# Performance work log

Hardware: AMD Instinct MI355X
Metric: run time of the kernel (lower is better)

Reference implementation:

```python
import jax, jax.numpy as jnp
import numpy as np

N, D, H, L, E, P = 50000, 128, 128, 3, 640000, 100000


def setup_inputs() -> dict:
    key = jax.random.key(0)
    ks = jax.random.split(key, 10)
    x = jax.random.normal(ks[0], (N, D), dtype=jnp.float32)
    ei = jax.random.randint(ks[1], (2, E), 0, N, dtype=jnp.int64)
    pos = jax.random.randint(ks[2], (2, P), 0, N, dtype=jnp.int64)
    neg = jax.random.randint(ks[3], (2, P), 0, N, dtype=jnp.int64)
    # GCN weights: layer0 is [D,H], rest [H,H]; D==H so stack as [L,H,H]
    gcn_w = jax.random.normal(ks[4], (L, H, H), dtype=jnp.float32) / np.sqrt(H)
    gcn_b = jnp.zeros((L, H), dtype=jnp.float32)
    pred_w = jax.random.normal(ks[5], (H * L, 1), dtype=jnp.float32) / np.sqrt(H * L)
    pred_b = jnp.zeros((1,), dtype=jnp.float32)
    return {"x": x, "ei": ei, "pos": pos, "neg": neg,
            "gcn_w": gcn_w, "gcn_b": gcn_b, "pred_w": pred_w, "pred_b": pred_b}


def reference(x, ei, pos, neg, gcn_w, gcn_b, pred_w, pred_b):
    n = x.shape[0]
    loops = jnp.arange(n, dtype=ei.dtype)
    src = jnp.concatenate([ei[0], loops])  # self-loops (GCNConv default)
    dst = jnp.concatenate([ei[1], loops])
    deg = jax.ops.segment_sum(jnp.ones_like(dst, dtype=x.dtype), dst, num_segments=n)
    dinv = jax.lax.rsqrt(deg)  # deg >= 1 thanks to self-loops
    coef = (dinv[src] * dinv[dst])[:, None]  # [E+N, 1] symmetric norm

    embs = []
    h = x
    for i in range(gcn_w.shape[0]):
        hw = h @ gcn_w[i]                                   # [N, H]
        agg = jax.ops.segment_sum(hw[src] * coef, dst, num_segments=n)
        h = jax.nn.relu(agg + gcn_b[i])
        embs.append(h)
    z = jnp.concatenate(embs, axis=1)                        # [N, H*L]

    def logits(e):
        return (z[e[0]] * z[e[1]]) @ pred_w + pred_b         # [P, 1]

    pos_logit = logits(pos)
    neg_logit = logits(neg)
    # BCEWithLogitsLoss with targets [1...1, 0...0], mean reduction
    total = pos_logit.shape[0] + neg_logit.shape[0]
    loss = (jnp.sum(-jax.nn.log_sigmoid(pos_logit)) +
            jnp.sum(-jax.nn.log_sigmoid(-neg_logit))) / total
    return loss
```

## Files before the change

### kernel.cpp

```cpp
#include <hip/hip_runtime.h>
#include <hip/hip_bf16.h>

#define DD 128

typedef __attribute__((ext_vector_type(8))) short short8;
typedef __attribute__((ext_vector_type(4))) float f32x4;
typedef __attribute__((ext_vector_type(2))) float f32x2;

static __device__ __forceinline__ int gtid() {
    return blockIdx.x * blockDim.x + threadIdx.x;
}

static __device__ __forceinline__ ushort f2bfu(float f) {
    __hip_bfloat16 h = __float2bfloat16(f);
    return *reinterpret_cast<ushort*>(&h);
}

static __device__ __forceinline__ unsigned int fp8e(float f) {
    unsigned int s = (__float_as_uint(f) >> 31) << 7;
    float a = fabsf(f);
    if (a < 0.015625f) return s | (unsigned int)rintf(a * 512.0f);
    unsigned int u = __float_as_uint(a);
    u += 0x0007FFFFu + ((u >> 20) & 1u);
    unsigned int e8 = (u >> 23) - 120u;
    unsigned int m = (u >> 20) & 7u;
    if (e8 > 15u || (e8 == 15u && m == 7u)) return s | 0x7Eu;
    return s | (e8 << 3) | m;
}

static __device__ __forceinline__ float fp8d(unsigned int b) {
    unsigned int t = b & 0x7Fu;
    float v = (t >= 8u) ? __uint_as_float((t << 20) + 0x3C000000u)
                        : (float)t * 0.001953125f;
    return (b & 0x80u) ? -v : v;
}

static __device__ __forceinline__ unsigned int pk8x2(float a, float b) {
#if __has_builtin(__builtin_amdgcn_cvt_pk_fp8_f32)
    return (unsigned int)__builtin_amdgcn_cvt_pk_fp8_f32(a, b, 0, false);
#else
    return fp8e(a) | (fp8e(b) << 8);
#endif
}

static __device__ __forceinline__ unsigned int pk8x4(float a, float b, float c, float d) {
#if __has_builtin(__builtin_amdgcn_cvt_pk_fp8_f32)
    int v = __builtin_amdgcn_cvt_pk_fp8_f32(a, b, 0, false);
    v = __builtin_amdgcn_cvt_pk_fp8_f32(c, d, v, true);
    return (unsigned int)v;
#else
    return fp8e(a) | (fp8e(b) << 8) | (fp8e(c) << 16) | (fp8e(d) << 24);
#endif
}

template <bool HI>
static __device__ __forceinline__ f32x2 fp8pk(unsigned int u) {
#if __has_builtin(__builtin_amdgcn_cvt_pk_f32_fp8)
    return __builtin_amdgcn_cvt_pk_f32_fp8((int)u, HI);
#else
    f32x2 r;
    unsigned int base = HI ? (u >> 16) : u;
    r[0] = fp8d(base & 0xFFu);
    r[1] = fp8d((base >> 8) & 0xFFu);
    return r;
#endif
}

#if __has_builtin(__builtin_elementwise_fma)
#define PKFMA(a, b, c) __builtin_elementwise_fma(a, b, c)
#else
static __device__ __forceinline__ f32x2 PKFMA(f32x2 a, f32x2 b, f32x2 c) {
    f32x2 r;
    r[0] = fmaf(a[0], b[0], c[0]);
    r[1] = fmaf(a[1], b[1], c[1]);
    return r;
}
#endif


__global__ void count_kernel(int* __restrict__ counts, const int* __restrict__ dst, int e) {
    int i = gtid();
    if (i < e) atomicAdd(&counts[dst[i]], 1);
}

__global__ __launch_bounds__(256) void scan_blocks(const int* __restrict__ counts,
                                                   int* __restrict__ rowptr,
                                                   int* __restrict__ partial,
                                                   float* __restrict__ dinv, int n) {
    __shared__ int s[256];
    int i = blockIdx.x * 256 + threadIdx.x;
    int v = (i < n) ? counts[i] : 0;
    if (i < n) dinv[i] = rsqrtf(1.0f + (float)v);
    s[threadIdx.x] = v;
    __syncthreads();
    for (int off = 1; off < 256; off <<= 1) {
        int t = (threadIdx.x >= off) ? s[threadIdx.x - off] : 0;
        __syncthreads();
        s[threadIdx.x] += t;
        __syncthreads();
    }
    if (i < n) rowptr[i] = s[threadIdx.x] - v;
    if (threadIdx.x == 255) partial[blockIdx.x] = s[255];
}

__global__ __launch_bounds__(256) void scan_partials(int* __restrict__ partial,
                                                     int* __restrict__ partial2, int nb) {
    __shared__ int s[256];
    int v = (threadIdx.x < nb) ? partial[threadIdx.x] : 0;
    s[threadIdx.x] = v;
    __syncthreads();
    for (int off = 1; off < 256; off <<= 1) {
        int t = (threadIdx.x >= off) ? s[threadIdx.x - off] : 0;
        __syncthreads();
        s[threadIdx.x] += t;
        __syncthreads();
    }
    partial2[threadIdx.x] = s[threadIdx.x] - v;
}

__global__ __launch_bounds__(256) void add_offsets(int* __restrict__ rowptr,
                                                   int* __restrict__ cursor,
                                                   const int* __restrict__ partial2,
                                                   int n, int e) {
    int i = blockIdx.x * 256 + threadIdx.x;
    if (i < n) {
        int r = rowptr[i] + partial2[blockIdx.x];
        rowptr[i] = r;
        cursor[i] = r;
        if (i == n - 1) rowptr[n] = e;
    }
}

__global__ __launch_bounds__(256) void fill_kernel(
    const int* __restrict__ ei, int* __restrict__ cursor,
    ushort* __restrict__ csr_src, int e, int n, int blocksPerPart) {
    int part = blockIdx.x & 7;
    int blk = blockIdx.x >> 3;
    int lo = (int)(((long)n * part) >> 3);
    int hi = (int)(((long)n * (part + 1)) >> 3);
    int stride = blocksPerPart * 256;
    for (int i = blk * 256 + threadIdx.x; i < e; i += stride) {
        int d = ei[e + i];
        if (d < lo || d >= hi) continue;
        int s = ei[i];
        int pos = atomicAdd(&cursor[d], 1);
        csr_src[pos] = (ushort)s;
    }
}

__global__ void cvt_kernel(const float* __restrict__ x, unsigned char* __restrict__ xq, size_t m8) {
    size_t i = (size_t)blockIdx.x * blockDim.x + threadIdx.x;
    if (i >= m8) return;
    const float4* xp = reinterpret_cast<const float4*>(x + i * 8);
    float4 a = xp[0], b = xp[1];
    uint2 q;
    q.x = pk8x4(a.x, a.y, a.z, a.w);
    q.y = pk8x4(b.x, b.y, b.z, b.w);
    *reinterpret_cast<uint2*>(xq + i * 8) = q;
}

__global__ __launch_bounds__(256) void wpack_kernel(const float* __restrict__ gcn_w,
                                                    ushort* __restrict__ wfrag) {
    int tid = blockIdx.x * 256 + threadIdx.x;
    if (tid >= 3 * 4 * 8 * 64) return;
    int lane = tid & 63;
    int c = (tid >> 6) & 7;
    int s = (tid >> 9) & 3;
    int l = tid >> 11;
    const float* W = gcn_w + (size_t)l * 128 * 128;
    int col = c * 16 + (lane & 15);
    int k0 = s * 32 + (lane >> 4) * 8;
    ushort u[8];
#pragma unroll
    for (int j = 0; j < 8; ++j) {
        u[j] = f2bfu(W[(size_t)(k0 + j) * 128 + col]);
    }
    *reinterpret_cast<uint4*>(wfrag + (size_t)tid * 8) = *reinterpret_cast<const uint4*>(u);
}

__global__ __launch_bounds__(1024) void layer_fused_kernel(
    const unsigned char* __restrict__ srcq, int srcStride,
    const int* __restrict__ rowptr, const ushort* __restrict__ csr_src,
    const float* __restrict__ dinv, const ushort* __restrict__ wfrag,
    const float* __restrict__ bias, const float* __restrict__ pwsl,
    unsigned char* __restrict__ zq_sl, unsigned char* __restrict__ zqw_sl, int n) {
    __shared__ unsigned char ah[16 * 256];
    int lane = threadIdx.x & 63;
    int wid = threadIdx.x >> 6;
    int row0 = blockIdx.x * 16;

    {
        int g = lane >> 3;
        int c = lane & 7;
        int row = row0 + wid;
        int j0 = rowptr[row], j1 = rowptr[row + 1];
        float dr = dinv[row];
        f32x2 acc2[8];
#pragma unroll
        for (int k = 0; k < 8; ++k) acc2[k] = (f32x2){0.f, 0.f};
        for (int j = j0 + g; j < j1; j += 8) {
            int s = (int)csr_src[j];
            float cf = dinv[s] * dr;
            f32x2 cf2 = {cf, cf};
            uint4 v = *reinterpret_cast<const uint4*>(srcq + (size_t)s * srcStride + c * 16);
            acc2[0] = PKFMA(cf2, fp8pk<false>(v.x), acc2[0]);
            acc2[1] = PKFMA(cf2, fp8pk<true>(v.x), acc2[1]);
            acc2[2] = PKFMA(cf2, fp8pk<false>(v.y), acc2[2]);
            acc2[3] = PKFMA(cf2, fp8pk<true>(v.y), acc2[3]);
            acc2[4] = PKFMA(cf2, fp8pk<false>(v.z), acc2[4]);
            acc2[5] = PKFMA(cf2, fp8pk<true>(v.z), acc2[5]);
            acc2[6] = PKFMA(cf2, fp8pk<false>(v.w), acc2[6]);
            acc2[7] = PKFMA(cf2, fp8pk<true>(v.w), acc2[7]);
        }
        {
            float d2 = dr * dr;
            f32x2 d22 = {d2, d2};
            uint4 sv = *reinterpret_cast<const uint4*>(srcq + (size_t)row * srcStride + c * 16);
            acc2[0] = PKFMA(d22, fp8pk<false>(sv.x), acc2[0]);
            acc2[1] = PKFMA(d22, fp8pk<true>(sv.x), acc2[1]);
            acc2[2] = PKFMA(d22, fp8pk<false>(sv.y), acc2[2]);
            acc2[3] = PKFMA(d22, fp8pk<true>(sv.y), acc2[3]);
            acc2[4] = PKFMA(d22, fp8pk<false>(sv.z), acc2[4]);
            acc2[5] = PKFMA(d22, fp8pk<true>(sv.z), acc2[5]);
            acc2[6] = PKFMA(d22, fp8pk<false>(sv.w), acc2[6]);
            acc2[7] = PKFMA(d22, fp8pk<true>(sv.w), acc2[7]);
        }
        float acc[16];
#pragma unroll
        for (int k = 0; k < 8; ++k) {
            acc[2 * k] = acc2[k][0];
            acc[2 * k + 1] = acc2[k][1];
        }
#pragma unroll
        for (int k = 0; k < 16; ++k) {
            acc[k] += __shfl_xor(acc[k], 8);
            acc[k] += __shfl_xor(acc[k], 16);
            acc[k] += __shfl_xor(acc[k], 32);
        }
        if (g == 0) {
            unsigned int pk[8];
#pragma unroll
            for (int q = 0; q < 8; ++q) {
                pk[q] = (unsigned int)f2bfu(acc[2 * q]) | ((unsigned int)f2bfu(acc[2 * q + 1]) << 16);
            }
            int swz = (wid & 7) << 4;
            int bo = c * 32;
            *reinterpret_cast<uint4*>(ah + wid * 256 + (bo ^ swz)) =
                *reinterpret_cast<const uint4*>(pk);
            *reinterpret_cast<uint4*>(ah + wid * 256 + ((bo + 16) ^ swz)) =
                *reinterpret_cast<const uint4*>(pk + 4);
        }
    }
    __syncthreads();
    if (wid >= 8) return;

    short8 bfr[4];
#pragma unroll
    for (int s = 0; s < 4; ++s) {
        bfr[s] = *reinterpret_cast<const short8*>(wfrag + ((size_t)(s * 8 + wid) * 64 + lane) * 8);
    }
    int rlo = lane & 15;
    int kg = lane >> 4;
    int swzr = (rlo & 7) << 4;
    const unsigned char* arow = ah + rlo * 256;
    short8 a0 = *reinterpret_cast<const short8*>(arow + ((kg * 16) ^ swzr));
    short8 a1 = *reinterpret_cast<const short8*>(arow + ((kg * 16 + 64) ^ swzr));
    short8 a2 = *reinterpret_cast<const short8*>(arow + ((kg * 16 + 128) ^ swzr));
    short8 a3 = *reinterpret_cast<const short8*>(arow + ((kg * 16 + 192) ^ swzr));
    f32x4 acc = {0.f, 0.f, 0.f, 0.f};
    acc = __builtin_amdgcn_mfma_f32_16x16x32_bf16(a0, bfr[0], acc, 0, 0, 0);
    acc = __builtin_amdgcn_mfma_f32_16x16x32_bf16(a1, bfr[1], acc, 0, 0, 0);
    acc = __builtin_amdgcn_mfma_f32_16x16x32_bf16(a2, bfr[2], acc, 0, 0, 0);
    acc = __builtin_amdgcn_mfma_f32_16x16x32_bf16(a3, bfr[3], acc, 0, 0, 0);

    int col = wid * 16 + rlo;
    float b0 = bias[col];
    float pw = pwsl[col] * 8.0f;
    int rowBase = row0 + kg * 4;
#pragma unroll
    for (int r = 0; r < 4; ++r) {
        float v = fmaxf(acc[r] + b0, 0.f);
        unsigned int q = pk8x2(v, v * pw);
        zq_sl[(size_t)(rowBase + r) * 384 + col] = (unsigned char)(q & 0xFFu);
        zqw_sl[(size_t)(rowBase + r) * 384 + col] = (unsigned char)((q >> 8) & 0xFFu);
    }
}

__global__ __launch_bounds__(256) void loss_mfma_kernel(
    const unsigned char* __restrict__ zq, const unsigned char* __restrict__ zqw,
    const int* __restrict__ pos, const int* __restrict__ neg,
    const float* __restrict__ pb, float* __restrict__ partialOut,
    int p, float inv_total) {
    __shared__ float red[4];
    int lane = threadIdx.x & 63;
    int wv = threadIdx.x >> 6;
    int pairBase = (blockIdx.x * 4 + wv) * 16;
    float term = 0.f;
    if (pairBase < 2 * p) {
        int m = lane & 15;
        int kg = lane >> 4;
        int pi = pairBase + m;
        int pic = (pi < 2 * p) ? pi : (2 * p - 1);
        bool isneg = (pic >= p);
        const int* pr = isneg ? neg : pos;
        int idx = isneg ? (pic - p) : pic;
        int a = pr[idx];
        int b = pr[p + idx];
        const long* pa = reinterpret_cast<const long*>(zq + (size_t)a * 384) + kg;
        const long* pbw = reinterpret_cast<const long*>(zqw + (size_t)b * 384) + kg;
        long av[12], bv[12];
#pragma unroll
        for (int s = 0; s < 12; ++s) av[s] = pa[s * 4];
#pragma unroll
        for (int s = 0; s < 12; ++s) bv[s] = pbw[s * 4];
        f32x4 acc = {0.f, 0.f, 0.f, 0.f};
#pragma unroll
        for (int s = 0; s < 12; ++s) {
            acc = __builtin_amdgcn_mfma_f32_16x16x32_fp8_fp8(av[s], bv[s], acc, 0, 0, 0);
        }
        bool isdiag = (lane >> 4) == ((lane & 15) >> 2);
        int r2 = lane & 3;
        float v = (r2 == 0) ? acc[0] : (r2 == 1) ? acc[1] : (r2 == 2) ? acc[2] : acc[3];
        if (isdiag && pi < 2 * p) {
            float logit = v * 0.125f + pb[0];
            float t = isneg ? logit : -logit;
            term = (fmaxf(t, 0.f) + log1pf(expf(-fabsf(t)))) * inv_total;
        }
    }
#pragma unroll
    for (int off = 1; off < 64; off <<= 1) term += __shfl_xor(term, off);
    if (lane == 0) red[wv] = term;
    __syncthreads();
    if (threadIdx.x == 0) partialOut[blockIdx.x] = red[0] + red[1] + red[2] + red[3];
}

__global__ __launch_bounds__(256) void loss_reduce_kernel(
    const float* __restrict__ partial, float* __restrict__ out, int m) {
    __shared__ float s[256];
    float a = 0.f;
    for (int i = threadIdx.x; i < m; i += 256) a += partial[i];
    s[threadIdx.x] = a;
    __syncthreads();
    for (int off = 128; off > 0; off >>= 1) {
        if (threadIdx.x < off) s[threadIdx.x] += s[threadIdx.x + off];
        __syncthreads();
    }
    if (threadIdx.x == 0) out[0] = s[0];
}

extern "C" void kernel_launch(void* const* d_in, const int* in_sizes, int n_in,
                              void* d_out, int out_size, void* d_ws, size_t ws_size,
                              hipStream_t stream) {
    const float* x      = (const float*)d_in[0];
    const int*   ei     = (const int*)d_in[1];
    const int*   pos    = (const int*)d_in[2];
    const int*   neg    = (const int*)d_in[3];
    const float* gcn_w  = (const float*)d_in[4];
    const float* gcn_b  = (const float*)d_in[5];
    const float* pred_w = (const float*)d_in[6];
    const float* pred_b = (const float*)d_in[7];
    float* out = (float*)d_out;

    const int n = in_sizes[0] / DD;
    const int e = in_sizes[1] / 2;
    const int p = in_sizes[2] / 2;
    const int nb = (n + 255) / 256;

    char* ws = (char*)d_ws;
    size_t off = 0;
    auto alloc = [&](size_t bytes) {
        void* ptr = ws + off;
        off += (bytes + 255) & ~(size_t)255;
        return ptr;
    };
    float* dinv      = (float*)alloc((size_t)n * 4);
    int*   counts    = (int*)alloc((size_t)n * 4);
    int*   rowptr    = (int*)alloc((size_t)(n + 1) * 4);
    int*   cursor    = (int*)alloc((size_t)n * 4);
    int*   partial   = (int*)alloc(256 * 4);
    int*   partial2  = (int*)alloc(256 * 4);
    float* lossPart  = (float*)alloc((size_t)4096 * 4);
    ushort* csr_src  = (ushort*)alloc((size_t)e * 2);
    ushort* wfrag    = (ushort*)alloc((size_t)3 * 2048 * 8 * 2);
    unsigned char* xq = (unsigned char*)alloc((size_t)n * 128);
    unsigned char* zq  = (unsigned char*)alloc((size_t)n * 384);
    unsigned char* zqw = (unsigned char*)alloc((size_t)n * 384);
    (void)ws_size;

    hipMemsetAsync(counts, 0, (size_t)n * 4, stream);

    count_kernel<<<(e + 255) / 256, 256, 0, stream>>>(counts, ei + e, e);
    scan_blocks<<<nb, 256, 0, stream>>>(counts, rowptr, partial, dinv, n);
    scan_partials<<<1, 256, 0, stream>>>(partial, partial2, nb);
    add_offsets<<<nb, 256, 0, stream>>>(rowptr, cursor, partial2, n, e);
    int blocksPerPart = (e + 255) / 256 / 2;
    fill_kernel<<<blocksPerPart * 8, 256, 0, stream>>>(ei, cursor, csr_src, e, n, blocksPerPart);

    size_t m8 = (size_t)n * 128 / 8;
    cvt_kernel<<<(int)((m8 + 255) / 256), 256, 0, stream>>>(x, xq, m8);
    wpack_kernel<<<24, 256, 0, stream>>>(gcn_w, wfrag);

    const int layerBlocks = n / 16;
    for (int l = 0; l < 3; ++l) {
        const unsigned char* srcq = (l == 0) ? xq : (zq + (size_t)(l - 1) * 128);
        int srcStride = (l == 0) ? 128 : 384;
        layer_fused_kernel<<<layerBlocks, 1024, 0, stream>>>(
            srcq, srcStride, rowptr, csr_src, dinv,
            wfrag + (size_t)l * 2048 * 8,
            gcn_b + (size_t)l * 128, pred_w + (size_t)l * 128,
            zq + (size_t)l * 128, zqw + (size_t)l * 128, n);
    }

    float inv_total = 1.0f / (2.0f * (float)p);
    int lossBlocks = (2 * p + 63) / 64;
    loss_mfma_kernel<<<lossBlocks, 256, 0, stream>>>(
        zq, zqw, pos, neg, pred_b, lossPart, p, inv_total);
    loss_reduce_kernel<<<1, 256, 0, stream>>>(lossPart, out, lossBlocks);
}
```

Baseline: 235.2 us.

## Sort nodes by in-degree so each 16-row block has balanced gather work

Builds a counting-sort permutation of nodes by in-degree (capped at 63) using a per-block histogram, a single-block scan and a stable scatter. The fused layer kernel then assigns each block 16 nodes of similar degree and writes outputs at the permuted row indices. The aim is to cut load imbalance, where one wave in a 1024-thread block processes a high-degree node while the other waves sit idle. The cost is three extra small kernel launches and scattered, non-contiguous output row writes, which may hurt locality.

```diff
diff --git a/kernel.cpp b/kernel.cpp
--- a/kernel.cpp
+++ b/kernel.cpp
@@ -148,6 +148,62 @@
     }
 }
 
+
+__global__ __launch_bounds__(256) void deg_hist_kernel(
+    const int* __restrict__ counts, int* __restrict__ histT, int n, int nb) {
+    __shared__ int h[64];
+    if (threadIdx.x < 64) h[threadIdx.x] = 0;
+    __syncthreads();
+    int i = blockIdx.x * 256 + threadIdx.x;
+    if (i < n) {
+        int bin = counts[i];
+        if (bin > 63) bin = 63;
+        atomicAdd(&h[bin], 1);
+    }
+    __syncthreads();
+    if (threadIdx.x < 64) histT[threadIdx.x * nb + blockIdx.x] = h[threadIdx.x];
+}
+
+__global__ __launch_bounds__(256) void hist_scan_kernel(int* __restrict__ data, int m) {
+    __shared__ int tot[256];
+    int chunk = (m + 255) / 256;
+    int lo = threadIdx.x * chunk;
+    int hi = lo + chunk;
+    if (hi > m) hi = m;
+    int sum = 0;
+    for (int i = lo; i < hi; ++i) sum += data[i];
+    tot[threadIdx.x] = sum;
+    __syncthreads();
+    for (int off = 1; off < 256; off <<= 1) {
+        int t = (threadIdx.x >= off) ? tot[threadIdx.x - off] : 0;
+        __syncthreads();
+        tot[threadIdx.x] += t;
+        __syncthreads();
+    }
+    int run = tot[threadIdx.x] - sum;
+    for (int i = lo; i < hi; ++i) {
+        int v = data[i];
+        data[i] = run;
+        run += v;
+    }
+}
+
+__global__ __launch_bounds__(256) void perm_scatter_kernel(
+    const int* __restrict__ counts, const int* __restrict__ histT,
+    int* __restrict__ perm, int n, int nb) {
+    __shared__ int cur[64];
+    int b = blockIdx.x;
+    if (threadIdx.x < 64) cur[threadIdx.x] = histT[threadIdx.x * nb + b];
+    __syncthreads();
+    int i = b * 256 + threadIdx.x;
+    if (i < n) {
+        int bin = counts[i];
+        if (bin > 63) bin = 63;
+        int pos = atomicAdd(&cur[bin], 1);
+        perm[pos] = i;
+    }
+}
+
 __global__ void cvt_kernel(const float* __restrict__ x, unsigned char* __restrict__ xq, size_t m8) {
     size_t i = (size_t)blockIdx.x * blockDim.x + threadIdx.x;
     if (i >= m8) return;
@@ -181,18 +237,22 @@
 __global__ __launch_bounds__(1024) void layer_fused_kernel(
     const unsigned char* __restrict__ srcq, int srcStride,
     const int* __restrict__ rowptr, const ushort* __restrict__ csr_src,
-    const float* __restrict__ dinv, const ushort* __restrict__ wfrag,
+    const float* __restrict__ dinv, const int* __restrict__ perm,
+    const ushort* __restrict__ wfrag,
     const float* __restrict__ bias, const float* __restrict__ pwsl,
     unsigned char* __restrict__ zq_sl, unsigned char* __restrict__ zqw_sl, int n) {
     __shared__ unsigned char ah[16 * 256];
+    __shared__ int ldsPerm[16];
     int lane = threadIdx.x & 63;
     int wid = threadIdx.x >> 6;
     int row0 = blockIdx.x * 16;
+    if (threadIdx.x < 16) ldsPerm[threadIdx.x] = perm[row0 + threadIdx.x];
+    __syncthreads();
 
     {
         int g = lane >> 3;
         int c = lane & 7;
-        int row = row0 + wid;
+        int row = ldsPerm[wid];
         int j0 = rowptr[row], j1 = rowptr[row + 1];
         float dr = dinv[row];
         f32x2 acc2[8];
@@ -276,13 +336,13 @@
     int col = wid * 16 + rlo;
     float b0 = bias[col];
     float pw = pwsl[col] * 8.0f;
-    int rowBase = row0 + kg * 4;
 #pragma unroll
     for (int r = 0; r < 4; ++r) {
+        int prow = ldsPerm[kg * 4 + r];
         float v = fmaxf(acc[r] + b0, 0.f);
         unsigned int q = pk8x2(v, v * pw);
-        zq_sl[(size_t)(rowBase + r) * 384 + col] = (unsigned char)(q & 0xFFu);
-        zqw_sl[(size_t)(rowBase + r) * 384 + col] = (unsigned char)((q >> 8) & 0xFFu);
+        zq_sl[(size_t)prow * 384 + col] = (unsigned char)(q & 0xFFu);
+        zqw_sl[(size_t)prow * 384 + col] = (unsigned char)((q >> 8) & 0xFFu);
     }
 }
 
@@ -380,6 +440,8 @@
     int*   partial   = (int*)alloc(256 * 4);
     int*   partial2  = (int*)alloc(256 * 4);
     float* lossPart  = (float*)alloc((size_t)4096 * 4);
+    int*   perm      = (int*)alloc((size_t)n * 4);
+    int*   histT     = (int*)alloc((size_t)64 * nb * 4);
     ushort* csr_src  = (ushort*)alloc((size_t)e * 2);
     ushort* wfrag    = (ushort*)alloc((size_t)3 * 2048 * 8 * 2);
     unsigned char* xq = (unsigned char*)alloc((size_t)n * 128);
@@ -396,6 +458,10 @@
     int blocksPerPart = (e + 255) / 256 / 2;
     fill_kernel<<<blocksPerPart * 8, 256, 0, stream>>>(ei, cursor, csr_src, e, n, blocksPerPart);
 
+    deg_hist_kernel<<<nb, 256, 0, stream>>>(counts, histT, n, nb);
+    hist_scan_kernel<<<1, 256, 0, stream>>>(histT, 64 * nb);
+    perm_scatter_kernel<<<nb, 256, 0, stream>>>(counts, histT, perm, n, nb);
+
     size_t m8 = (size_t)n * 128 / 8;
     cvt_kernel<<<(int)((m8 + 255) / 256), 256, 0, stream>>>(x, xq, m8);
     wpack_kernel<<<24, 256, 0, stream>>>(gcn_w, wfrag);
@@ -405,7 +471,7 @@
         const unsigned char* srcq = (l == 0) ? xq : (zq + (size_t)(l - 1) * 128);
         int srcStride = (l == 0) ? 128 : 384;
         layer_fused_kernel<<<layerBlocks, 1024, 0, stream>>>(
-            srcq, srcStride, rowptr, csr_src, dinv,
+            srcq, srcStride, rowptr, csr_src, dinv, perm,
             wfrag + (size_t)l * 2048 * 8,
             gcn_b + (size_t)l * 128, pred_w + (size_t)l * 128,
             zq + (size_t)l * 128, zqw + (size_t)l * 128, n);
```

Result: slower. 280.4 us (+19.2%).
